# Optimization experiments

Measured on AMD Instinct MI355X. Metric: run time of the kernel, lower is better.

Reference implementation:

```python
import jax, jax.numpy as jnp
import numpy as np
from jax import lax

EPS = 1e-5

def _layernorm_c(x, w, b):
    # WithBias LayerNorm over channel dim (to_3d puts C last; equivalent to axis=1 here)
    mu = x.mean(axis=1, keepdims=True)
    var = x.var(axis=1, keepdims=True)
    return (x - mu) / jnp.sqrt(var + EPS) * w[None, :, None, None] + b[None, :, None, None]

def _conv1x1(x, W, b=None):
    y = jnp.einsum('bchw,oc->bohw', x, W)
    if b is not None:
        y = y + b[None, :, None, None]
    return y

def _dwconv3x3(x, k):
    # k: [C, 1, 3, 3], groups = C
    return lax.conv_general_dilated(
        x, k, window_strides=(1, 1), padding='SAME',
        dimension_numbers=('NCHW', 'OIHW', 'NCHW'),
        feature_group_count=k.shape[0])

def setup_inputs() -> dict:
    key = jax.random.key(0)
    B, C, H, W = 4, 128, 96, 256
    ks = jax.random.split(key, 12)
    s = 0.05
    return {
        'x_l': jax.random.normal(ks[0], (B, C, H, W), jnp.float32),
        'x_r': jax.random.normal(ks[1], (B, C, H, W), jnp.float32),
        'Wl_m': jax.random.normal(ks[2], (2 * C, C), jnp.float32) * s,
        'Wr_m': jax.random.normal(ks[3], (2 * C, C), jnp.float32) * s,
        'dw_l': jax.random.normal(ks[4], (2 * C, 1, 3, 3), jnp.float32) * s,
        'dw_r': jax.random.normal(ks[5], (2 * C, 1, 3, 3), jnp.float32) * s,
        'lnl_w': jnp.ones((C,), jnp.float32),
        'lnl_b': jnp.zeros((C,), jnp.float32),
        'lnr_w': jnp.ones((C,), jnp.float32),
        'lnr_b': jnp.zeros((C,), jnp.float32),
        'Wq_l': jax.random.normal(ks[6], (C, C), jnp.float32) * s,
        'bq_l': jnp.zeros((C,), jnp.float32),
        'Wq_r': jax.random.normal(ks[7], (C, C), jnp.float32) * s,
        'bq_r': jnp.zeros((C,), jnp.float32),
        'beta': jax.random.normal(ks[8], (1, C, 1, 1), jnp.float32) * s,
        'gamma': jax.random.normal(ks[9], (1, C, 1, 1), jnp.float32) * s,
    }

def reference(x_l, x_r, Wl_m, Wr_m, dw_l, dw_r, lnl_w, lnl_b, lnr_w, lnr_b,
              Wq_l, bq_l, Wq_r, bq_r, beta, gamma):
    c = x_l.shape[1]
    scale = c ** -0.5
    fusion_l = _dwconv3x3(_conv1x1(x_l, Wl_m), dw_l)   # [b,2c,h,w]
    V_l, l_mid = jnp.split(fusion_l, 2, axis=1)
    fusion_r = _dwconv3x3(_conv1x1(x_r, Wr_m), dw_r)
    V_r, r_mid = jnp.split(fusion_r, 2, axis=1)
    Q_l = _conv1x1(_layernorm_c(l_mid, lnl_w, lnl_b), Wq_l, bq_l)  # [b,c,h,w]
    Q_r = _conv1x1(_layernorm_c(r_mid, lnr_w, lnr_b), Wq_r, bq_r)  # [b,c,h,w]
    # row-wise attention over width: [b,h,w,w]
    attn = jnp.einsum('bchw,bchv->bhwv', Q_l, Q_r) * scale
    # F_r2l: softmax over last axis (v), contract V_r over v
    F_r2l = jnp.einsum('bhwv,bchv->bchw', jax.nn.softmax(attn, axis=-1), V_r)
    # F_l2r: softmax of attn^T over its last axis == softmax over w (axis=-2)
    F_l2r = jnp.einsum('bhwv,bchw->bchv', jax.nn.softmax(attn, axis=-2), V_l)
    out_l = x_l + F_r2l * beta
    out_r = x_r + F_l2r * gamma
    return (out_l, out_r)
```

## Files before the change

kernel.cpp:

```cpp
#include <hip/hip_runtime.h>
#include <hip/hip_bf16.h>

using bf16 = __hip_bfloat16;
typedef __attribute__((ext_vector_type(8))) short bf16x8;
typedef __attribute__((ext_vector_type(2))) float f32x2;
typedef __attribute__((ext_vector_type(4))) float f32x4;
typedef __attribute__((ext_vector_type(16))) float f32x16;
typedef __attribute__((ext_vector_type(4))) unsigned int u32x4;

#define DEVI __device__ __forceinline__

constexpr int B = 4, C = 128, C2 = 256, H = 96, W = 256;
constexpr int HW = H * W;
constexpr int NPIX = B * HW;
constexpr int BH = B * H;
constexpr float SCALE = 0.08838834764831845f;
constexpr float LN_EPS = 1e-5f;

DEVI float lo16(unsigned u) { return __builtin_bit_cast(float, u << 16); }
DEVI float hi16(unsigned u) { return __builtin_bit_cast(float, u & 0xffff0000u); }
DEVI unsigned short f2bu(float v) {
    bf16 b = __float2bfloat16(v);
    return __builtin_bit_cast(unsigned short, b);
}
DEVI unsigned packbf2(float a, float b) {
    return (unsigned)f2bu(a) | ((unsigned)f2bu(b) << 16);
}
DEVI f32x2 up2(unsigned p) { return f32x2{lo16(p), hi16(p)}; }

__global__ __launch_bounds__(256) void wcvt_kernel(
    const float* __restrict__ w0, const float* __restrict__ w1,
    const float* __restrict__ w2, const float* __restrict__ w3,
    unsigned short* __restrict__ o0, unsigned short* __restrict__ o1,
    unsigned short* __restrict__ o2, unsigned short* __restrict__ o3)
{
    const int id = blockIdx.x, t = threadIdx.x;
    const float* src; unsigned short* dst; int base;
    if (id < 8)       { src = w0; dst = o0; base = id * 4096; }
    else if (id < 16) { src = w1; dst = o1; base = (id - 8) * 4096; }
    else if (id < 20) { src = w2; dst = o2; base = (id - 16) * 4096; }
    else              { src = w3; dst = o3; base = (id - 20) * 4096; }
#pragma unroll
    for (int u = 0; u < 4; ++u) {
        int i = base + t * 16 + u * 4;
        float4 v = *reinterpret_cast<const float4*>(&src[i]);
        ushort4 o;
        o.x = f2bu(v.x); o.y = f2bu(v.y); o.z = f2bu(v.z); o.w = f2bu(v.w);
        *reinterpret_cast<ushort4*>(&dst[i]) = o;
    }
}

__global__ __launch_bounds__(256) void transpose_kernel(
    const float* __restrict__ x_l, const float* __restrict__ x_r,
    unsigned short* __restrict__ xT_l, unsigned short* __restrict__ xT_r)
{
    __shared__ unsigned short ts[64][132];
    const int side = blockIdx.x & 1;
    const int u = blockIdx.x >> 1;
    const float* x = side ? x_r : x_l;
    unsigned short* xT = side ? xT_r : xT_l;
    const int t = threadIdx.x;
    const int b = u / (HW / 64);
    const int hw0 = (u % (HW / 64)) * 64;
#pragma unroll
    for (int i = 0; i < 8; ++i) {
        int idx = t + i * 256;
        int c = idx >> 4;
        int px = (idx & 15) * 4;
        float4 v = *reinterpret_cast<const float4*>(&x[((size_t)b * C + c) * HW + hw0 + px]);
        ts[px + 0][c] = f2bu(v.x);
        ts[px + 1][c] = f2bu(v.y);
        ts[px + 2][c] = f2bu(v.z);
        ts[px + 3][c] = f2bu(v.w);
    }
    __syncthreads();
#pragma unroll
    for (int i = 0; i < 8; ++i) {
        int idx = t + i * 256;
        int px = idx >> 5;
        int c4 = (idx & 31) * 4;
        ushort4 v = *reinterpret_cast<const ushort4*>(&ts[px][c4]);
        *reinterpret_cast<ushort4*>(&xT[(size_t)(b * HW + hw0 + px) * C + c4]) = v;
    }
}

__global__ __launch_bounds__(256) void conv1x1_mfma_kernel(
    const unsigned short* __restrict__ xT_l, const unsigned short* __restrict__ xT_r,
    const unsigned short* __restrict__ Wb_l, const unsigned short* __restrict__ Wb_r,
    unsigned short* __restrict__ y_l, unsigned short* __restrict__ y_r)
{
    const int side = blockIdx.x & 1;
    const int u = blockIdx.x >> 1;
    const unsigned short* xT = side ? xT_r : xT_l;
    const unsigned short* Wb = side ? Wb_r : Wb_l;
    unsigned short* y = side ? y_r : y_l;

    const int t = threadIdx.x;
    const int lane = t & 63, wid = t >> 6;
    const int wr = wid >> 1, wc = wid & 1;
    const int l15 = lane & 15, l4 = lane >> 4;
    const int pxb = u % 768;
    const int ocb = u / 768;

    const int px_base = pxb * 128 + wr * 64 + l15;
    const int oc_base = ocb * 128 + wc * 64 + l15;

    f32x4 acc[4][4] = {};
    for (int kk = 0; kk < 4; ++kk) {
        const int k0 = kk * 32 + l4 * 8;
        bf16x8 a[4], bb[4];
#pragma unroll
        for (int mt = 0; mt < 4; ++mt)
            a[mt] = *reinterpret_cast<const bf16x8*>(&xT[(size_t)(px_base + mt * 16) * C + k0]);
#pragma unroll
        for (int nt = 0; nt < 4; ++nt)
            bb[nt] = *reinterpret_cast<const bf16x8*>(&Wb[(size_t)(oc_base + nt * 16) * C + k0]);
#pragma unroll
        for (int mt = 0; mt < 4; ++mt)
#pragma unroll
            for (int nt = 0; nt < 4; ++nt)
                acc[mt][nt] = __builtin_amdgcn_mfma_f32_16x16x32_bf16(a[mt], bb[nt], acc[mt][nt], 0, 0, 0);
    }
#pragma unroll
    for (int mt = 0; mt < 4; ++mt)
#pragma unroll
        for (int nt = 0; nt < 4; ++nt) {
            const int oc = ocb * 128 + wc * 64 + nt * 16 + l15;
#pragma unroll
            for (int r = 0; r < 4; ++r) {
                const int px = pxb * 128 + wr * 64 + mt * 16 + l4 * 4 + r;
                y[(size_t)px * C2 + oc] = f2bu(acc[mt][nt][r]);
            }
        }
}

__global__ __launch_bounds__(256) void dwlnq_kernel(
    const unsigned short* __restrict__ y_l, const unsigned short* __restrict__ y_r,
    const float* __restrict__ dwk_l, const float* __restrict__ dwk_r,
    const float* __restrict__ lnw_l, const float* __restrict__ lnb_l,
    const float* __restrict__ lnw_r, const float* __restrict__ lnb_r,
    const unsigned short* __restrict__ Wq_l, const unsigned short* __restrict__ Wq_r,
    const float* __restrict__ bq_l, const float* __restrict__ bq_r,
    unsigned short* __restrict__ VT_l, unsigned short* __restrict__ VT_r,
    unsigned short* __restrict__ q_l, unsigned short* __restrict__ q_r)
{
    __shared__ unsigned char msb[64 * 256];

    const int side = blockIdx.x & 1;
    const int u = blockIdx.x >> 1;
    const unsigned short* y = side ? y_r : y_l;
    const float* dwk = side ? dwk_r : dwk_l;
    const float* lnw = side ? lnw_r : lnw_l;
    const float* lnb = side ? lnb_r : lnb_l;
    const unsigned short* Wqb = side ? Wq_r : Wq_l;
    const float* bq = side ? bq_r : bq_l;
    unsigned short* VT = side ? VT_r : VT_l;
    unsigned short* q = side ? q_r : q_l;

    const int t = threadIdx.x;
    const int wt = u & 3;
    const int bh = u >> 2;
    const int h = bh % H;
    const int ch8 = t & 31, wi = t >> 5;
    const int c0 = ch8 * 8;
    const int wbase = wt * 64 + wi * 8;

    f32x2 acc2[8][4] = {};
#pragma unroll
    for (int dh = 0; dh < 3; ++dh) {
        const int hh = h + dh - 1;
        if ((unsigned)hh >= (unsigned)H) continue;
        f32x2 wt0[4], wt1[4], wt2[4];
#pragma unroll
        for (int k = 0; k < 4; ++k) {
            const float* d0 = dwk + (c0 + 2 * k) * 9 + dh * 3;
            const float* d1 = dwk + (c0 + 2 * k + 1) * 9 + dh * 3;
            wt0[k] = f32x2{d0[0], d1[0]};
            wt1[k] = f32x2{d0[1], d1[1]};
            wt2[k] = f32x2{d0[2], d1[2]};
        }
        const unsigned short* yrow = y + (size_t)(bh + dh - 1) * W * C2 + c0;
        uint4 uu[10];
#pragma unroll
        for (int j = 0; j < 10; ++j) {
            const int ww = wbase - 1 + j;
            uint4 v = {0u, 0u, 0u, 0u};
            if ((unsigned)ww < 256u)
                v = *reinterpret_cast<const uint4*>(&yrow[(size_t)ww * C2]);
            uu[j] = v;
        }
#pragma unroll
        for (int j = 0; j < 10; ++j) {
            const unsigned arr[4] = {uu[j].x, uu[j].y, uu[j].z, uu[j].w};
            f32x2 v[4];
#pragma unroll
            for (int k = 0; k < 4; ++k) v[k] = up2(arr[k]);
            if (j < 8) {
#pragma unroll
                for (int k = 0; k < 4; ++k) acc2[j][k] += v[k] * wt0[k];
            }
            if (j >= 1 && j <= 8) {
#pragma unroll
                for (int k = 0; k < 4; ++k) acc2[j - 1][k] += v[k] * wt1[k];
            }
            if (j >= 2) {
#pragma unroll
                for (int k = 0; k < 4; ++k) acc2[j - 2][k] += v[k] * wt2[k];
            }
        }
    }

    if (c0 < 128) {
#pragma unroll
        for (int k = 0; k < 8; ++k) {
            uint4 o;
            o.x = packbf2(acc2[0][k >> 1][k & 1], acc2[1][k >> 1][k & 1]);
            o.y = packbf2(acc2[2][k >> 1][k & 1], acc2[3][k >> 1][k & 1]);
            o.z = packbf2(acc2[4][k >> 1][k & 1], acc2[5][k >> 1][k & 1]);
            o.w = packbf2(acc2[6][k >> 1][k & 1], acc2[7][k >> 1][k & 1]);
            *reinterpret_cast<uint4*>(&VT[((size_t)bh * C + c0 + k) * W + wbase]) = o;
        }
    } else {
        float s1[8], s2[8];
#pragma unroll
        for (int i = 0; i < 8; ++i) {
            float a = 0.f, b2 = 0.f;
#pragma unroll
            for (int k = 0; k < 4; ++k) {
                a  += acc2[i][k].x + acc2[i][k].y;
                b2 += acc2[i][k].x * acc2[i][k].x + acc2[i][k].y * acc2[i][k].y;
            }
            s1[i] = a; s2[i] = b2;
        }
#pragma unroll
        for (int off = 1; off <= 8; off <<= 1)
#pragma unroll
            for (int i = 0; i < 8; ++i) {
                s1[i] += __shfl_xor(s1[i], off);
                s2[i] += __shfl_xor(s2[i], off);
            }
        const int cm = c0 - 128;
        float lw[8], lb[8];
        {
            float4 a0 = *reinterpret_cast<const float4*>(&lnw[cm]);
            float4 a1 = *reinterpret_cast<const float4*>(&lnw[cm + 4]);
            float4 b0 = *reinterpret_cast<const float4*>(&lnb[cm]);
            float4 b1 = *reinterpret_cast<const float4*>(&lnb[cm + 4]);
            lw[0] = a0.x; lw[1] = a0.y; lw[2] = a0.z; lw[3] = a0.w;
            lw[4] = a1.x; lw[5] = a1.y; lw[6] = a1.z; lw[7] = a1.w;
            lb[0] = b0.x; lb[1] = b0.y; lb[2] = b0.z; lb[3] = b0.w;
            lb[4] = b1.x; lb[5] = b1.y; lb[6] = b1.z; lb[7] = b1.w;
        }
#pragma unroll
        for (int i = 0; i < 8; ++i) {
            const float mu = s1[i] * (1.f / C);
            const float rs = rsqrtf(s2[i] * (1.f / C) - mu * mu + LN_EPS);
            float nv[8];
#pragma unroll
            for (int k = 0; k < 4; ++k) {
                nv[k * 2]     = (acc2[i][k].x - mu) * rs * lw[k * 2] + lb[k * 2];
                nv[k * 2 + 1] = (acc2[i][k].y - mu) * rs * lw[k * 2 + 1] + lb[k * 2 + 1];
            }
            uint4 o;
            o.x = packbf2(nv[0], nv[1]); o.y = packbf2(nv[2], nv[3]);
            o.z = packbf2(nv[4], nv[5]); o.w = packbf2(nv[6], nv[7]);
            const int pxl = wi * 8 + i;
            const unsigned addr =
                (unsigned)(pxl * 256 + cm * 2) ^ (unsigned)((pxl & 7) << 4);
            *reinterpret_cast<uint4*>(msb + addr) = o;
        }
    }
    __syncthreads();

    {
        const int lane = t & 63, wid = t >> 6;
        const int l15 = lane & 15, l4 = lane >> 4;
        f32x4 acc[8] = {};
        for (int kk = 0; kk < 4; ++kk) {
            const int k0 = kk * 32 + l4 * 8;
            const int pxl = wid * 16 + l15;
            const unsigned aaddr =
                (unsigned)(pxl * 256 + k0 * 2) ^ (unsigned)((pxl & 7) << 4);
            bf16x8 a = *reinterpret_cast<const bf16x8*>(msb + aaddr);
#pragma unroll
            for (int nt = 0; nt < 8; ++nt) {
                bf16x8 bv = *reinterpret_cast<const bf16x8*>(
                    &Wqb[(size_t)(nt * 16 + l15) * C + k0]);
                acc[nt] = __builtin_amdgcn_mfma_f32_16x16x32_bf16(a, bv, acc[nt], 0, 0, 0);
            }
        }
        const size_t px0 = (size_t)bh * W + wt * 64;
#pragma unroll
        for (int nt = 0; nt < 8; ++nt) {
            const int oc = nt * 16 + l15;
            const float bias = bq[oc];
#pragma unroll
            for (int r = 0; r < 4; ++r) {
                const int pxr = wid * 16 + l4 * 4 + r;
                q[(px0 + pxr) * C + oc] = f2bu(acc[nt][r] + bias);
            }
        }
    }
}

__global__ __launch_bounds__(256, 2) void fused_attn_kernel(
    const unsigned short* __restrict__ Q_l, const unsigned short* __restrict__ Q_r,
    const unsigned short* __restrict__ VT_l, const unsigned short* __restrict__ VT_r,
    const float* __restrict__ x_l, const float* __restrict__ x_r,
    const float* __restrict__ beta, const float* __restrict__ gamma,
    float* __restrict__ out_l, float* __restrict__ out_r)
{
    __shared__ __align__(16) unsigned char lds[65536];
    const int bid = blockIdx.x;
    const int xcd = bid & 7;
    const int local = bid >> 3;
    const int bh = xcd * 48 + (local >> 2);
    const int sub = local & 3;
    const int side = sub & 1, half = sub >> 1;

    const unsigned short* Q  = side ? Q_r : Q_l;
    const unsigned short* K  = side ? Q_l : Q_r;
    const unsigned short* VT = side ? VT_l : VT_r;
    const float* x    = side ? x_r : x_l;
    const float* coef = side ? gamma : beta;
    float* out        = side ? out_r : out_l;

    const int t = threadIdx.x;
    const int lane = t & 63, wv = t >> 6;
    const int l31 = lane & 31, hi = lane >> 5;
    const int b = bh / H, h = bh % H;
    const int w0 = half * 128 + wv * 32;

    const unsigned short* qrow = Q + ((size_t)bh * W + w0 + l31) * C + hi * 8;
    bf16x8 qfrag[8];
#pragma unroll
    for (int ks = 0; ks < 8; ++ks)
        qfrag[ks] = *reinterpret_cast<const bf16x8*>(qrow + ks * 16);

    const char* kg = (const char*)(K + (size_t)bh * W * C);
    const char* vg = (const char*)(VT + (size_t)bh * C * W);
    const int srow = lane >> 4;
    const int scol = (lane & 15) * 16;

    float sden_loc = 0.f;
    f32x16 oacc[4] = {};

    for (int ci = 0; ci < 2; ++ci) {
#pragma unroll
        for (int i = 0; i < 8; ++i) {
            const int r0 = wv * 32 + i * 4;
            const int row = r0 + srow;
            const char* src = kg + (size_t)(ci * 128 + row) * 256 + (scol ^ ((row & 7) << 4));
            __builtin_amdgcn_global_load_lds(
                (const __attribute__((address_space(1))) void*)src,
                (__attribute__((address_space(3))) void*)(lds + r0 * 256), 16, 0, 0);
        }
#pragma unroll
        for (int i = 0; i < 8; ++i) {
            const int r0 = wv * 32 + i * 4;
            const int row = r0 + srow;
            const char* src = vg + (size_t)row * 512 + ci * 256 + (scol ^ ((row & 7) << 4));
            __builtin_amdgcn_global_load_lds(
                (const __attribute__((address_space(1))) void*)src,
                (__attribute__((address_space(3))) void*)(lds + 32768 + r0 * 256), 16, 0, 0);
        }
        __syncthreads();

        f32x16 sacc[4] = {};
        __builtin_amdgcn_s_setprio(1);
#pragma unroll
        for (int vt = 0; vt < 4; ++vt) {
            const int row = vt * 32 + l31;
            const unsigned rb = row * 256;
            const unsigned sw = (row & 7) << 4;
#pragma unroll
            for (int ks = 0; ks < 8; ++ks) {
                bf16x8 a = *reinterpret_cast<const bf16x8*>(
                    lds + rb + ((ks * 32 + hi * 16) ^ sw));
                sacc[vt] = __builtin_amdgcn_mfma_f32_32x32x16_bf16(a, qfrag[ks], sacc[vt], 0, 0, 0);
            }
        }
        __builtin_amdgcn_s_setprio(0);

#pragma unroll
        for (int vt = 0; vt < 4; ++vt)
#pragma unroll
            for (int r = 0; r < 16; ++r) {
                float e = __expf(sacc[vt][r] * SCALE);
                sacc[vt][r] = e;
                sden_loc += e;
            }

        unsigned pw[8][4];
#pragma unroll
        for (int g = 0; g < 8; ++g) {
            const int vt = g >> 1, bs = (g & 1) * 8;
            unsigned pa = packbf2(sacc[vt][bs + 0], sacc[vt][bs + 1]);
            unsigned pc = packbf2(sacc[vt][bs + 2], sacc[vt][bs + 3]);
            unsigned pb = packbf2(sacc[vt][bs + 4], sacc[vt][bs + 5]);
            unsigned pd = packbf2(sacc[vt][bs + 6], sacc[vt][bs + 7]);
            unsigned sa = __shfl_xor(pa, 32);
            unsigned sb = __shfl_xor(pb, 32);
            unsigned sc = __shfl_xor(pc, 32);
            unsigned sd = __shfl_xor(pd, 32);
            pw[g][0] = hi ? sb : pa;
            pw[g][1] = hi ? sd : pc;
            pw[g][2] = hi ? pb : sa;
            pw[g][3] = hi ? pd : sc;
        }

        __builtin_amdgcn_s_setprio(1);
#pragma unroll
        for (int ct = 0; ct < 4; ++ct) {
            const int row = ct * 32 + l31;
            const unsigned rb = 32768 + row * 256;
            const unsigned sw = (row & 7) << 4;
#pragma unroll
            for (int g = 0; g < 8; ++g) {
                bf16x8 va = *reinterpret_cast<const bf16x8*>(
                    lds + rb + ((g * 32 + hi * 16) ^ sw));
                u32x4 pv = {pw[g][0], pw[g][1], pw[g][2], pw[g][3]};
                oacc[ct] = __builtin_amdgcn_mfma_f32_32x32x16_bf16(
                    va, __builtin_bit_cast(bf16x8, pv), oacc[ct], 0, 0, 0);
            }
        }
        __builtin_amdgcn_s_setprio(0);
        __syncthreads();
    }

    const float sden = sden_loc + __shfl_xor(sden_loc, 32);
    const float inv = 1.f / sden;
    const size_t base0 = (size_t)b * C * HW + (size_t)h * W + w0 + l31;
#pragma unroll
    for (int ct = 0; ct < 4; ++ct)
#pragma unroll
        for (int r = 0; r < 16; ++r) {
            const int c = ct * 32 + (r & 3) + 8 * (r >> 2) + 4 * hi;
            const size_t a = base0 + (size_t)c * HW;
            out[a] = x[a] + oacc[ct][r] * inv * coef[c];
        }
}

extern "C" void kernel_launch(void* const* d_in, const int* in_sizes, int n_in,
                              void* d_out, int out_size, void* d_ws, size_t ws_size,
                              hipStream_t stream) {
    (void)in_sizes; (void)n_in; (void)out_size; (void)ws_size;
    const float* x_l   = (const float*)d_in[0];
    const float* x_r   = (const float*)d_in[1];
    const float* Wl_m  = (const float*)d_in[2];
    const float* Wr_m  = (const float*)d_in[3];
    const float* dw_l  = (const float*)d_in[4];
    const float* dw_r  = (const float*)d_in[5];
    const float* lnl_w = (const float*)d_in[6];
    const float* lnl_b = (const float*)d_in[7];
    const float* lnr_w = (const float*)d_in[8];
    const float* lnr_b = (const float*)d_in[9];
    const float* Wq_l  = (const float*)d_in[10];
    const float* bq_l  = (const float*)d_in[11];
    const float* Wq_r  = (const float*)d_in[12];
    const float* bq_r  = (const float*)d_in[13];
    const float* beta  = (const float*)d_in[14];
    const float* gamma = (const float*)d_in[15];

    char* ws = (char*)d_ws;
    unsigned short* ymid_l   = (unsigned short*)(ws + 0);
    unsigned short* ymid_r   = (unsigned short*)(ws + 50331648);
    unsigned short* VT_l     = (unsigned short*)(ws + 150994944);
    unsigned short* VT_r     = (unsigned short*)(ws + 176160768);
    unsigned short* Q_l      = (unsigned short*)(ws + 201326592);
    unsigned short* Q_r      = (unsigned short*)(ws + 226492416);
    unsigned short* Wlb      = (unsigned short*)(ws + 251658240);
    unsigned short* Wrb      = (unsigned short*)(ws + 251723776);
    unsigned short* Wqlb     = (unsigned short*)(ws + 251789312);
    unsigned short* Wqrb     = (unsigned short*)(ws + 251822080);
    unsigned short* xT_l     = Q_l;
    unsigned short* xT_r     = Q_r;

    float* out_l = (float*)d_out;
    float* out_r = out_l + (size_t)B * C * HW;

    const dim3 blk(256);

    wcvt_kernel<<<24, blk, 0, stream>>>(Wl_m, Wr_m, Wq_l, Wq_r, Wlb, Wrb, Wqlb, Wqrb);

    transpose_kernel<<<3072, blk, 0, stream>>>(x_l, x_r, xT_l, xT_r);
    conv1x1_mfma_kernel<<<3072, blk, 0, stream>>>(xT_l, xT_r, Wlb, Wrb, ymid_l, ymid_r);
    dwlnq_kernel<<<3072, blk, 0, stream>>>(ymid_l, ymid_r, dw_l, dw_r,
                                           lnl_w, lnl_b, lnr_w, lnr_b,
                                           Wqlb, Wqrb, bq_l, bq_r,
                                           VT_l, VT_r, Q_l, Q_r);
    fused_attn_kernel<<<1536, blk, 0, stream>>>(Q_l, Q_r, VT_l, VT_r,
                                                x_l, x_r, beta, gamma, out_l, out_r);
}
```

Measured before the change: 255.3 us.

## Vectorize conv1x1/Q stores via swapped MFMA operands and widen dwlnq blocks

The conv1x1 and Q-projection MFMAs swap their A/B operands, so each lane holds four consecutive output channels for one pixel. This lets results be written as packed 8-byte stores instead of scattered 2-byte stores into the channel-last layouts. The depthwise/LayerNorm/Q kernel now runs 512 threads per block, each handling 4 pixels instead of 8, and the Q projection is split across 8 waves by pixel group and output half. This lowers per-thread register pressure and raises parallelism, at the cost of more halo reloads in the depthwise stage.

```diff
diff --git a/kernel.cpp b/kernel.cpp
--- a/kernel.cpp
+++ b/kernel.cpp
@@ -119,22 +119,23 @@
         for (int mt = 0; mt < 4; ++mt)
 #pragma unroll
             for (int nt = 0; nt < 4; ++nt)
-                acc[mt][nt] = __builtin_amdgcn_mfma_f32_16x16x32_bf16(a[mt], bb[nt], acc[mt][nt], 0, 0, 0);
-    }
-#pragma unroll
-    for (int mt = 0; mt < 4; ++mt)
+                acc[mt][nt] = __builtin_amdgcn_mfma_f32_16x16x32_bf16(bb[nt], a[mt], acc[mt][nt], 0, 0, 0);
+    }
+#pragma unroll
+    for (int mt = 0; mt < 4; ++mt) {
+        const int px = pxb * 128 + wr * 64 + mt * 16 + l15;
 #pragma unroll
         for (int nt = 0; nt < 4; ++nt) {
-            const int oc = ocb * 128 + wc * 64 + nt * 16 + l15;
-#pragma unroll
-            for (int r = 0; r < 4; ++r) {
-                const int px = pxb * 128 + wr * 64 + mt * 16 + l4 * 4 + r;
-                y[(size_t)px * C2 + oc] = f2bu(acc[mt][nt][r]);
-            }
-        }
-}
-
-__global__ __launch_bounds__(256) void dwlnq_kernel(
+            const int oc = ocb * 128 + wc * 64 + nt * 16 + l4 * 4;
+            uint2 o;
+            o.x = packbf2(acc[mt][nt][0], acc[mt][nt][1]);
+            o.y = packbf2(acc[mt][nt][2], acc[mt][nt][3]);
+            *reinterpret_cast<uint2*>(&y[(size_t)px * C2 + oc]) = o;
+        }
+    }
+}
+
+__global__ __launch_bounds__(512) void dwlnq_kernel(
     const unsigned short* __restrict__ y_l, const unsigned short* __restrict__ y_r,
     const float* __restrict__ dwk_l, const float* __restrict__ dwk_r,
     const float* __restrict__ lnw_l, const float* __restrict__ lnb_l,
@@ -161,11 +162,11 @@
     const int wt = u & 3;
     const int bh = u >> 2;
     const int h = bh % H;
-    const int ch8 = t & 31, wi = t >> 5;
+    const int ch8 = t & 31, pg = t >> 5;
     const int c0 = ch8 * 8;
-    const int wbase = wt * 64 + wi * 8;
-
-    f32x2 acc2[8][4] = {};
+    const int wbase = wt * 64 + pg * 4;
+
+    f32x2 acc2[4][4] = {};
 #pragma unroll
     for (int dh = 0; dh < 3; ++dh) {
         const int hh = h + dh - 1;
@@ -180,9 +181,9 @@
             wt2[k] = f32x2{d0[2], d1[2]};
         }
         const unsigned short* yrow = y + (size_t)(bh + dh - 1) * W * C2 + c0;
-        uint4 uu[10];
-#pragma unroll
-        for (int j = 0; j < 10; ++j) {
+        uint4 uu[6];
+#pragma unroll
+        for (int j = 0; j < 6; ++j) {
             const int ww = wbase - 1 + j;
             uint4 v = {0u, 0u, 0u, 0u};
             if ((unsigned)ww < 256u)
@@ -190,16 +191,16 @@
             uu[j] = v;
         }
 #pragma unroll
-        for (int j = 0; j < 10; ++j) {
+        for (int j = 0; j < 6; ++j) {
             const unsigned arr[4] = {uu[j].x, uu[j].y, uu[j].z, uu[j].w};
             f32x2 v[4];
 #pragma unroll
             for (int k = 0; k < 4; ++k) v[k] = up2(arr[k]);
-            if (j < 8) {
+            if (j < 4) {
 #pragma unroll
                 for (int k = 0; k < 4; ++k) acc2[j][k] += v[k] * wt0[k];
             }
-            if (j >= 1 && j <= 8) {
+            if (j >= 1 && j <= 4) {
 #pragma unroll
                 for (int k = 0; k < 4; ++k) acc2[j - 1][k] += v[k] * wt1[k];
             }
@@ -213,17 +214,15 @@
     if (c0 < 128) {
 #pragma unroll
         for (int k = 0; k < 8; ++k) {
-            uint4 o;
+            uint2 o;
             o.x = packbf2(acc2[0][k >> 1][k & 1], acc2[1][k >> 1][k & 1]);
             o.y = packbf2(acc2[2][k >> 1][k & 1], acc2[3][k >> 1][k & 1]);
-            o.z = packbf2(acc2[4][k >> 1][k & 1], acc2[5][k >> 1][k & 1]);
-            o.w = packbf2(acc2[6][k >> 1][k & 1], acc2[7][k >> 1][k & 1]);
-            *reinterpret_cast<uint4*>(&VT[((size_t)bh * C + c0 + k) * W + wbase]) = o;
+            *reinterpret_cast<uint2*>(&VT[((size_t)bh * C + c0 + k) * W + wbase]) = o;
         }
     } else {
-        float s1[8], s2[8];
-#pragma unroll
-        for (int i = 0; i < 8; ++i) {
+        float s1[4], s2[4];
+#pragma unroll
+        for (int i = 0; i < 4; ++i) {
             float a = 0.f, b2 = 0.f;
 #pragma unroll
             for (int k = 0; k < 4; ++k) {
@@ -235,7 +234,7 @@
 #pragma unroll
         for (int off = 1; off <= 8; off <<= 1)
 #pragma unroll
-            for (int i = 0; i < 8; ++i) {
+            for (int i = 0; i < 4; ++i) {
                 s1[i] += __shfl_xor(s1[i], off);
                 s2[i] += __shfl_xor(s2[i], off);
             }
@@ -252,7 +251,7 @@
             lb[4] = b1.x; lb[5] = b1.y; lb[6] = b1.z; lb[7] = b1.w;
         }
 #pragma unroll
-        for (int i = 0; i < 8; ++i) {
+        for (int i = 0; i < 4; ++i) {
             const float mu = s1[i] * (1.f / C);
             const float rs = rsqrtf(s2[i] * (1.f / C) - mu * mu + LN_EPS);
             float nv[8];
@@ -264,7 +263,7 @@
             uint4 o;
             o.x = packbf2(nv[0], nv[1]); o.y = packbf2(nv[2], nv[3]);
             o.z = packbf2(nv[4], nv[5]); o.w = packbf2(nv[6], nv[7]);
-            const int pxl = wi * 8 + i;
+            const int pxl = pg * 4 + i;
             const unsigned addr =
                 (unsigned)(pxl * 256 + cm * 2) ^ (unsigned)((pxl & 7) << 4);
             *reinterpret_cast<uint4*>(msb + addr) = o;
@@ -275,30 +274,30 @@
     {
         const int lane = t & 63, wid = t >> 6;
         const int l15 = lane & 15, l4 = lane >> 4;
-        f32x4 acc[8] = {};
+        const int rowg = wid & 3, oh = wid >> 2;
+        f32x4 acc[4] = {};
         for (int kk = 0; kk < 4; ++kk) {
             const int k0 = kk * 32 + l4 * 8;
-            const int pxl = wid * 16 + l15;
+            const int pxl = rowg * 16 + l15;
             const unsigned aaddr =
                 (unsigned)(pxl * 256 + k0 * 2) ^ (unsigned)((pxl & 7) << 4);
             bf16x8 a = *reinterpret_cast<const bf16x8*>(msb + aaddr);
 #pragma unroll
-            for (int nt = 0; nt < 8; ++nt) {
+            for (int nt = 0; nt < 4; ++nt) {
                 bf16x8 bv = *reinterpret_cast<const bf16x8*>(
-                    &Wqb[(size_t)(nt * 16 + l15) * C + k0]);
-                acc[nt] = __builtin_amdgcn_mfma_f32_16x16x32_bf16(a, bv, acc[nt], 0, 0, 0);
-            }
-        }
-        const size_t px0 = (size_t)bh * W + wt * 64;
-#pragma unroll
-        for (int nt = 0; nt < 8; ++nt) {
-            const int oc = nt * 16 + l15;
-            const float bias = bq[oc];
-#pragma unroll
-            for (int r = 0; r < 4; ++r) {
-                const int pxr = wid * 16 + l4 * 4 + r;
-                q[(px0 + pxr) * C + oc] = f2bu(acc[nt][r] + bias);
-            }
+                    &Wqb[(size_t)(oh * 64 + nt * 16 + l15) * C + k0]);
+                acc[nt] = __builtin_amdgcn_mfma_f32_16x16x32_bf16(bv, a, acc[nt], 0, 0, 0);
+            }
+        }
+        const size_t pxg = (size_t)bh * W + wt * 64 + rowg * 16 + l15;
+#pragma unroll
+        for (int nt = 0; nt < 4; ++nt) {
+            const int oc = oh * 64 + nt * 16 + l4 * 4;
+            const float4 bias = *reinterpret_cast<const float4*>(&bq[oc]);
+            uint2 o;
+            o.x = packbf2(acc[nt][0] + bias.x, acc[nt][1] + bias.y);
+            o.y = packbf2(acc[nt][2] + bias.z, acc[nt][3] + bias.w);
+            *reinterpret_cast<uint2*>(&q[pxg * C + oc]) = o;
         }
     }
 }
@@ -485,10 +484,10 @@
 
     transpose_kernel<<<3072, blk, 0, stream>>>(x_l, x_r, xT_l, xT_r);
     conv1x1_mfma_kernel<<<3072, blk, 0, stream>>>(xT_l, xT_r, Wlb, Wrb, ymid_l, ymid_r);
-    dwlnq_kernel<<<3072, blk, 0, stream>>>(ymid_l, ymid_r, dw_l, dw_r,
-                                           lnl_w, lnl_b, lnr_w, lnr_b,
-                                           Wqlb, Wqrb, bq_l, bq_r,
-                                           VT_l, VT_r, Q_l, Q_r);
+    dwlnq_kernel<<<3072, dim3(512), 0, stream>>>(ymid_l, ymid_r, dw_l, dw_r,
+                                                 lnl_w, lnl_b, lnr_w, lnr_b,
+                                                 Wqlb, Wqrb, bq_l, bq_r,
+                                                 VT_l, VT_r, Q_l, Q_r);
     fused_attn_kernel<<<1536, blk, 0, stream>>>(Q_l, Q_r, VT_l, VT_r,
                                                 x_l, x_r, beta, gamma, out_l, out_r);
 }
```

After: 285.9 us. 12.0% more time.
